# Optimization experiments

Measured on AMD Instinct MI355X. Metric: run time of the kernel, lower is better.

The kernel has to match this reference:

```python
import jax, jax.numpy as jnp
import numpy as np

N_NODES = 100000
N_EDGES = 1600000
N_FEAT = 128
HIDDEN = 64
N_CLASSES = 40


def setup_inputs() -> dict:
    key = jax.random.key(0)
    ks = jax.random.split(key, 4)
    x = jax.random.normal(ks[0], (N_NODES, N_FEAT), dtype=jnp.float32)
    edge_index = jax.random.randint(ks[1], (2, N_EDGES), 0, N_NODES, dtype=jnp.int64)
    # Glorot-style init like PyG GCNConv
    W1 = jax.random.normal(ks[2], (N_FEAT, HIDDEN), dtype=jnp.float32) * (1.0 / np.sqrt(N_FEAT))
    b1 = jnp.zeros((HIDDEN,), dtype=jnp.float32)
    W2 = jax.random.normal(ks[3], (HIDDEN, N_CLASSES), dtype=jnp.float32) * (1.0 / np.sqrt(HIDDEN))
    b2 = jnp.zeros((N_CLASSES,), dtype=jnp.float32)
    return {"x": x, "edge_index": edge_index, "W1": W1, "b1": b1, "W2": W2, "b2": b2}


def _gcn_conv(x, src, dst, norm, W, b, n_nodes):
    # PyG GCNConv: transform first, then normalized scatter-add aggregation
    h = x @ W                                   # [N, out]
    msg = h[src] * norm[:, None]                # [E+N, out] gather
    out = jax.ops.segment_sum(msg, dst, num_segments=n_nodes)  # scatter-add
    return out + b


def _norm_and_loops(edge_index, n_nodes):
    # add self-loops, symmetric normalization deg^{-1/2} A_hat deg^{-1/2}
    loop = jnp.arange(n_nodes, dtype=edge_index.dtype)
    src = jnp.concatenate([edge_index[0], loop])
    dst = jnp.concatenate([edge_index[1], loop])
    deg = jax.ops.segment_sum(jnp.ones_like(dst, dtype=jnp.float32), dst, num_segments=n_nodes)
    dinv = jnp.where(deg > 0, jax.lax.rsqrt(jnp.maximum(deg, 1.0)), 0.0)
    norm = dinv[src] * dinv[dst]
    return src, dst, norm


def reference(x, edge_index, W1, b1, W2, b2):
    n_nodes = x.shape[0]
    src, dst, norm = _norm_and_loops(edge_index, n_nodes)
    h = _gcn_conv(x, src, dst, norm, W1, b1, n_nodes)
    h = jax.nn.relu(h)
    h = _gcn_conv(h, src, dst, norm, W2, b2, n_nodes)
    return jax.nn.log_softmax(h, axis=1)
```

## Files before the change

### kernel.cpp

```cpp
#include <hip/hip_runtime.h>
#include <hip/hip_bf16.h>
#include <string.h>

#define N_FEAT 128
#define HIDDEN 64
#define N_CLS  40
#define FILL_BLOCKS 2048
#define CHUNK_EDGES 1024
#define B_BITS 6
#define SRC_BITS 17

typedef __bf16 bf16x8 __attribute__((ext_vector_type(8)));
typedef float  f32x4  __attribute__((ext_vector_type(4)));

union Frag { unsigned u[4]; bf16x8 v; };

static __device__ inline int get_xcc() {
    return (int)(__builtin_amdgcn_s_getreg((3 << 11) | 20) & 7u);
}


static __device__ inline unsigned pack_bf16(float a, float b) {
    unsigned ba = __float_as_uint(a);
    unsigned bb = __float_as_uint(b);
    unsigned ra = (ba + 0x7fffu + ((ba >> 16) & 1u)) >> 16;
    unsigned rb = (bb + 0x7fffu + ((bb >> 16) & 1u)) >> 16;
    return (ra & 0xffffu) | (rb << 16);
}

static __device__ inline float2 unpack_bf16(unsigned v) {
    return make_float2(__uint_as_float(v << 16), __uint_as_float(v & 0xffff0000u));
}


__global__ void detect_layout_kernel(const int* __restrict__ ei, int* __restrict__ flag) {
    int lane = threadIdx.x;
    int v = ei[2 * lane + 1];
    unsigned long long b = __ballot(v != 0);
    if (lane == 0) flag[0] = (b == 0ull) ? 1 : 0;
}


__global__ __launch_bounds__(256) void bucket_hist_kernel(const int* __restrict__ ei,
                                                          const int* __restrict__ flag,
                                                          unsigned* __restrict__ bcnt,
                                                          int E, int nbuk) {
    __shared__ unsigned h[2048];
    for (int i = threadIdx.x; i < nbuk; i += 256) h[i] = 0u;
    __syncthreads();
    bool is64 = (flag[0] != 0);
    if (is64) {
        int idx = blockIdx.x * 256 + threadIdx.x;
        int stride2 = gridDim.x * 256 * 2;
        int Eeven = E & ~1;
        for (int e = idx * 2; e < Eeven; e += stride2) {
            uint4 dv = *(const uint4*)(ei + (size_t)2 * E + (size_t)2 * e);
            atomicAdd(&h[((int)dv.x) >> B_BITS], 1u);
            atomicAdd(&h[((int)dv.z) >> B_BITS], 1u);
        }
        for (int e = Eeven + idx; e < E; e += gridDim.x * 256) {
            int d = ei[(size_t)2 * E + (size_t)2 * e];
            atomicAdd(&h[d >> B_BITS], 1u);
        }
    } else {
        const int* dstp = ei + E;
        for (int e = blockIdx.x * 256 + threadIdx.x; e < E; e += gridDim.x * 256) {
            int d = dstp[e];
            atomicAdd(&h[d >> B_BITS], 1u);
        }
    }
    __syncthreads();
    for (int i = threadIdx.x; i < nbuk; i += 256)
        if (h[i]) atomicAdd(&bcnt[i], h[i]);
}


__global__ __launch_bounds__(512) void bucket_scan_kernel(const unsigned* __restrict__ bcnt,
                                                          unsigned* __restrict__ bbase,
                                                          unsigned* __restrict__ bcur, int nbuk) {
    __shared__ unsigned tmp[512];
    __shared__ unsigned carry;
    if (threadIdx.x == 0) carry = 0u;
    __syncthreads();
    for (int base = 0; base < nbuk; base += 512) {
        int i = base + threadIdx.x;
        unsigned v = (i < nbuk) ? bcnt[i] : 0u;
        tmp[threadIdx.x] = v;
        __syncthreads();
#pragma unroll
        for (int off = 1; off < 512; off <<= 1) {
            unsigned t = (threadIdx.x >= (unsigned)off) ? tmp[threadIdx.x - off] : 0u;
            __syncthreads();
            tmp[threadIdx.x] += t;
            __syncthreads();
        }
        unsigned excl = tmp[threadIdx.x] - v + carry;
        if (i < nbuk) {
            bbase[i] = excl;
            bcur[(size_t)i * 16] = excl;
        }
        __syncthreads();
        if (threadIdx.x == 511) carry += tmp[511];
        __syncthreads();
    }
}


static __device__ inline void fill_edge(unsigned s, int d, int blo, int bhi,
                                        unsigned* bcur, unsigned* tmpbuf) {
    int b = d >> B_BITS;
    if (b >= blo && b < bhi) {
        unsigned val = s | ((unsigned)(d & ((1 << B_BITS) - 1)) << SRC_BITS);
        unsigned slot = __hip_atomic_fetch_add(&bcur[(size_t)b * 16], 1u, __ATOMIC_RELAXED,
                                               __HIP_MEMORY_SCOPE_WORKGROUP);
        tmpbuf[slot] = val;
    }
}

__global__ __launch_bounds__(256) void fill_buckets_kernel(const int* __restrict__ ei,
                                                           const int* __restrict__ flag,
                                                           unsigned* __restrict__ bcur,
                                                           unsigned* __restrict__ ctr,
                                                           unsigned* __restrict__ tmpbuf,
                                                           int E, int nbuk) {
    int r = get_xcc();
    int bpx = (nbuk + 7) >> 3;
    int blo = r * bpx;
    int bhi = min(nbuk, blo + bpx);
    bool is64 = (flag[0] != 0);
    const int* dstp = is64 ? (ei + 2 * E) : (ei + E);
    int stride = is64 ? 2 : 1;
    __shared__ unsigned chunk_s;
    for (;;) {
        if (threadIdx.x == 0)
            chunk_s = __hip_atomic_fetch_add(&ctr[r * 64], 1u, __ATOMIC_RELAXED,
                                             __HIP_MEMORY_SCOPE_WORKGROUP);
        __syncthreads();
        long long base = (long long)chunk_s * CHUNK_EDGES;
        __syncthreads();
        if (base >= E) break;
        if (is64 && base + CHUNK_EDGES <= E) {
            int e0 = (int)base + threadIdx.x * 2;
            int e1 = e0 + 512;
            uint4 sA = *(const uint4*)(ei + (size_t)2 * e0);
            uint4 sB = *(const uint4*)(ei + (size_t)2 * e1);
            uint4 dA = *(const uint4*)(ei + (size_t)2 * E + (size_t)2 * e0);
            uint4 dB = *(const uint4*)(ei + (size_t)2 * E + (size_t)2 * e1);
            fill_edge(sA.x, (int)dA.x, blo, bhi, bcur, tmpbuf);
            fill_edge(sA.z, (int)dA.z, blo, bhi, bcur, tmpbuf);
            fill_edge(sB.x, (int)dB.x, blo, bhi, bcur, tmpbuf);
            fill_edge(sB.z, (int)dB.z, blo, bhi, bcur, tmpbuf);
        } else {
            int end = (int)min((long long)E, base + CHUNK_EDGES);
            for (int e = (int)base + threadIdx.x; e < end; e += 256) {
                int d = dstp[(size_t)e * stride];
                int b = d >> B_BITS;
                if (b >= blo && b < bhi) {
                    int s = ei[(size_t)e * stride];
                    unsigned val = (unsigned)s | ((unsigned)(d & ((1 << B_BITS) - 1)) << SRC_BITS);
                    unsigned slot = __hip_atomic_fetch_add(&bcur[(size_t)b * 16], 1u, __ATOMIC_RELAXED,
                                                           __HIP_MEMORY_SCOPE_WORKGROUP);
                    tmpbuf[slot] = val;
                }
            }
        }
    }
}


__global__ __launch_bounds__(256) void bucket_to_csr_kernel(const unsigned* __restrict__ tmpbuf,
                                                            const unsigned* __restrict__ bbase,
                                                            unsigned* __restrict__ deg,
                                                            unsigned* __restrict__ rowptr,
                                                            float* __restrict__ dinv,
                                                            int* __restrict__ csr_src,
                                                            int nbuk, int N, int E) {
    int b = blockIdx.x;
    int tid = threadIdx.x;
    unsigned beg = bbase[b];
    unsigned end = (b + 1 < nbuk) ? bbase[b + 1] : (unsigned)E;
    int d0 = b << B_BITS;
    const int ND = 1 << B_BITS;
    __shared__ unsigned hist[ND], scn[ND], cur[ND];
    if (tid < ND) { hist[tid] = 0u; cur[tid] = 0u; }
    __syncthreads();
    for (unsigned i = beg + tid; i < end; i += 256)
        atomicAdd(&hist[tmpbuf[i] >> SRC_BITS], 1u);
    __syncthreads();
    if (tid == 0) {
        unsigned run = 0;
        for (int k = 0; k < ND; ++k) { scn[k] = run; run += hist[k]; }
    }
    __syncthreads();
    if (tid < ND) {
        int d = d0 + tid;
        if (d < N) {
            unsigned dg = hist[tid];
            deg[d] = dg;
            dinv[d] = rsqrtf((float)(dg + 1u));
            rowptr[d] = beg + scn[tid];
        }
    }
    __syncthreads();
    for (unsigned i = beg + tid; i < end; i += 256) {
        unsigned v = tmpbuf[i];
        unsigned dl = v >> SRC_BITS;
        unsigned s = v & ((1u << SRC_BITS) - 1u);
        unsigned p = atomicAdd(&cur[dl], 1u);
        csr_src[beg + scn[dl] + p] = (int)s;
    }
}


__global__ __launch_bounds__(256) void gemm1_mfma_kernel(const float* __restrict__ x,
                                                         const float* __restrict__ W1,
                                                         unsigned* __restrict__ h1b, int N) {
    int lane = threadIdx.x & 63;
    int quad = lane >> 4;
    int col  = lane & 15;

    Frag B[4][4];
#pragma unroll
    for (int c = 0; c < 4; ++c)
#pragma unroll
        for (int ks = 0; ks < 4; ++ks) {
            int n = c * 16 + col;
#pragma unroll
            for (int jj = 0; jj < 4; ++jj) {
                int k = ks * 32 + quad * 8 + 2 * jj;
                B[c][ks].u[jj] = pack_bf16(W1[k * HIDDEN + n], W1[(k + 1) * HIDDEN + n]);
            }
        }

    int wave_id = blockIdx.x * 4 + (threadIdx.x >> 6);
    int nwaves  = gridDim.x * 4;
    int ntiles  = (N + 15) >> 4;

    for (int rt = wave_id; rt < ntiles; rt += nwaves) {
        int rowA = rt * 16 + col;
        Frag A[4];
#pragma unroll
        for (int ks = 0; ks < 4; ++ks) {
            float4 a0 = make_float4(0.f, 0.f, 0.f, 0.f), a1 = a0;
            if (rowA < N) {
                const float4* ap = (const float4*)(x + (size_t)rowA * N_FEAT + ks * 32 + quad * 8);
                a0 = ap[0];
                a1 = ap[1];
            }
            A[ks].u[0] = pack_bf16(a0.x, a0.y);
            A[ks].u[1] = pack_bf16(a0.z, a0.w);
            A[ks].u[2] = pack_bf16(a1.x, a1.y);
            A[ks].u[3] = pack_bf16(a1.z, a1.w);
        }
        f32x4 acc[4] = {{0.f, 0.f, 0.f, 0.f}, {0.f, 0.f, 0.f, 0.f},
                        {0.f, 0.f, 0.f, 0.f}, {0.f, 0.f, 0.f, 0.f}};
#pragma unroll
        for (int ks = 0; ks < 4; ++ks)
#pragma unroll
            for (int c = 0; c < 4; ++c)
                acc[c] = __builtin_amdgcn_mfma_f32_16x16x32_bf16(A[ks].v, B[c][ks].v, acc[c], 0, 0, 0);

        int rowD = rt * 16 + quad * 4;
#pragma unroll
        for (int c = 0; c < 4; ++c)
#pragma unroll
            for (int r = 0; r < 4; ++r) {
                float v = acc[c][r];
                float nxt = __shfl_down(v, 1);
                int row = rowD + r;
                if (((lane & 1) == 0) && row < N)
                    h1b[(size_t)row * 32 + ((c * 16 + col) >> 1)] = pack_bf16(v, nxt);
            }
    }
}


__global__ __launch_bounds__(256) void gemm2_mfma_kernel(const unsigned* __restrict__ actb,
                                                         const float* __restrict__ W2,
                                                         unsigned* __restrict__ h2b, int N) {
    int lane = threadIdx.x & 63;
    int quad = lane >> 4;
    int col  = lane & 15;

    Frag B[3][2];
#pragma unroll
    for (int c = 0; c < 3; ++c)
#pragma unroll
        for (int ks = 0; ks < 2; ++ks) {
            int n = c * 16 + col;
#pragma unroll
            for (int jj = 0; jj < 4; ++jj) {
                int k = ks * 32 + quad * 8 + 2 * jj;
                float w0 = (n < N_CLS) ? W2[k * N_CLS + n] : 0.f;
                float w1 = (n < N_CLS) ? W2[(k + 1) * N_CLS + n] : 0.f;
                B[c][ks].u[jj] = pack_bf16(w0, w1);
            }
        }

    int wave_id = blockIdx.x * 4 + (threadIdx.x >> 6);
    int nwaves  = gridDim.x * 4;
    int ntiles  = (N + 15) >> 4;

    for (int rt = wave_id; rt < ntiles; rt += nwaves) {
        int rowA = rt * 16 + col;
        Frag A[2];
#pragma unroll
        for (int ks = 0; ks < 2; ++ks) {
            uint4 u = make_uint4(0u, 0u, 0u, 0u);
            if (rowA < N)
                u = *(const uint4*)(actb + (size_t)rowA * 32 + ks * 16 + quad * 4);
            A[ks].u[0] = u.x; A[ks].u[1] = u.y; A[ks].u[2] = u.z; A[ks].u[3] = u.w;
        }
        f32x4 acc[3] = {{0.f, 0.f, 0.f, 0.f}, {0.f, 0.f, 0.f, 0.f}, {0.f, 0.f, 0.f, 0.f}};
#pragma unroll
        for (int ks = 0; ks < 2; ++ks)
#pragma unroll
            for (int c = 0; c < 3; ++c)
                acc[c] = __builtin_amdgcn_mfma_f32_16x16x32_bf16(A[ks].v, B[c][ks].v, acc[c], 0, 0, 0);

        int rowD = rt * 16 + quad * 4;
#pragma unroll
        for (int c = 0; c < 3; ++c)
#pragma unroll
            for (int r = 0; r < 4; ++r) {
                float v = acc[c][r];
                float nxt = __shfl_down(v, 1);
                int row = rowD + r;
                int pair = (c * 16 + col) >> 1;
                if (((lane & 1) == 0) && pair < 20 && row < N)
                    h2b[(size_t)row * 20 + pair] = pack_bf16(v, nxt);
            }
    }
}


__global__ __launch_bounds__(256) void agg1_kernel(const unsigned* __restrict__ h1b,
                                                   const int* __restrict__ csr_src,
                                                   const unsigned* __restrict__ rowptr,
                                                   const unsigned* __restrict__ deg,
                                                   const float* __restrict__ dinv,
                                                   const float* __restrict__ b1,
                                                   unsigned* __restrict__ actb, int N) {
    int wave = threadIdx.x >> 6, lane = threadIdx.x & 63;
    int sub = lane >> 5, j = lane & 31;
    int d = blockIdx.x * 4 + wave;
    if (d >= N) return;
    float dv = dinv[d];
    float acc0 = 0.f, acc1 = 0.f;
    if (sub == 0) {
        float2 v = unpack_bf16(h1b[(size_t)d * 32 + j]);
        acc0 = dv * v.x; acc1 = dv * v.y;
    }
    unsigned beg = rowptr[d];
    int len = (int)deg[d];
    int i = 0;
    for (; i + 8 <= len; i += 8) {
        int s0 = csr_src[beg + i + sub];
        int s1 = csr_src[beg + i + 2 + sub];
        int s2 = csr_src[beg + i + 4 + sub];
        int s3 = csr_src[beg + i + 6 + sub];
        float w0 = dinv[s0], w1 = dinv[s1], w2 = dinv[s2], w3 = dinv[s3];
        unsigned v0 = h1b[(size_t)s0 * 32 + j];
        unsigned v1 = h1b[(size_t)s1 * 32 + j];
        unsigned v2 = h1b[(size_t)s2 * 32 + j];
        unsigned v3 = h1b[(size_t)s3 * 32 + j];
        float2 a0 = unpack_bf16(v0), a1 = unpack_bf16(v1);
        float2 a2 = unpack_bf16(v2), a3 = unpack_bf16(v3);
        acc0 += w0 * a0.x + w1 * a1.x + w2 * a2.x + w3 * a3.x;
        acc1 += w0 * a0.y + w1 * a1.y + w2 * a2.y + w3 * a3.y;
    }
    for (; i + 4 <= len; i += 4) {
        int sA = csr_src[beg + i + sub];
        int sB = csr_src[beg + i + 2 + sub];
        float wA = dinv[sA], wB = dinv[sB];
        float2 a = unpack_bf16(h1b[(size_t)sA * 32 + j]);
        float2 b = unpack_bf16(h1b[(size_t)sB * 32 + j]);
        acc0 += wA * a.x + wB * b.x;
        acc1 += wA * a.y + wB * b.y;
    }
    for (; i < len; i += 2) {
        int e = i + sub;
        if (e < len) {
            int s = csr_src[beg + e];
            float w = dinv[s];
            float2 a = unpack_bf16(h1b[(size_t)s * 32 + j]);
            acc0 += w * a.x;
            acc1 += w * a.y;
        }
    }
    acc0 += __shfl_xor(acc0, 32);
    acc1 += __shfl_xor(acc1, 32);
    if (sub == 0) {
        float2 bb = ((const float2*)b1)[j];
        float r0 = fmaxf(acc0 * dv + bb.x, 0.f);
        float r1 = fmaxf(acc1 * dv + bb.y, 0.f);
        actb[(size_t)d * 32 + j] = pack_bf16(r0, r1);
    }
}


__global__ __launch_bounds__(256) void agg2_lsm_kernel(const unsigned* __restrict__ h2b,
                                                       const int* __restrict__ csr_src,
                                                       const unsigned* __restrict__ rowptr,
                                                       const unsigned* __restrict__ deg,
                                                       const float* __restrict__ dinv,
                                                       const float* __restrict__ b2,
                                                       float* __restrict__ out, int N) {
    int wave = threadIdx.x >> 6, lane = threadIdx.x & 63;
    int sub = lane >> 5, j = lane & 31;
    bool act = (j < 20);
    int d = blockIdx.x * 4 + wave;
    if (d >= N) return;
    float dv = dinv[d];
    float acc0 = 0.f, acc1 = 0.f;
    if (sub == 0 && act) {
        float2 v = unpack_bf16(h2b[(size_t)d * 20 + j]);
        acc0 = dv * v.x; acc1 = dv * v.y;
    }
    unsigned beg = rowptr[d];
    int len = (int)deg[d];
    int i = 0;
    for (; i + 8 <= len; i += 8) {
        int s0 = csr_src[beg + i + sub];
        int s1 = csr_src[beg + i + 2 + sub];
        int s2 = csr_src[beg + i + 4 + sub];
        int s3 = csr_src[beg + i + 6 + sub];
        float w0 = dinv[s0], w1 = dinv[s1], w2 = dinv[s2], w3 = dinv[s3];
        if (act) {
            float2 a0 = unpack_bf16(h2b[(size_t)s0 * 20 + j]);
            float2 a1 = unpack_bf16(h2b[(size_t)s1 * 20 + j]);
            float2 a2 = unpack_bf16(h2b[(size_t)s2 * 20 + j]);
            float2 a3 = unpack_bf16(h2b[(size_t)s3 * 20 + j]);
            acc0 += w0 * a0.x + w1 * a1.x + w2 * a2.x + w3 * a3.x;
            acc1 += w0 * a0.y + w1 * a1.y + w2 * a2.y + w3 * a3.y;
        }
    }
    for (; i + 4 <= len; i += 4) {
        int sA = csr_src[beg + i + sub];
        int sB = csr_src[beg + i + 2 + sub];
        float wA = dinv[sA], wB = dinv[sB];
        if (act) {
            float2 a = unpack_bf16(h2b[(size_t)sA * 20 + j]);
            float2 b = unpack_bf16(h2b[(size_t)sB * 20 + j]);
            acc0 += wA * a.x + wB * b.x;
            acc1 += wA * a.y + wB * b.y;
        }
    }
    for (; i < len; i += 2) {
        int e = i + sub;
        if (e < len && act) {
            int s = csr_src[beg + e];
            float w = dinv[s];
            float2 a = unpack_bf16(h2b[(size_t)s * 20 + j]);
            acc0 += w * a.x;
            acc1 += w * a.y;
        }
    }
    acc0 += __shfl_xor(acc0, 32);
    acc1 += __shfl_xor(acc1, 32);
    float v0 = -1e30f, v1 = -1e30f;
    if (act) {
        float2 bb = ((const float2*)b2)[j];
        v0 = acc0 * dv + bb.x;
        v1 = acc1 * dv + bb.y;
    }
    float m = fmaxf(v0, v1);
#pragma unroll
    for (int off = 32; off > 0; off >>= 1)
        m = fmaxf(m, __shfl_xor(m, off));
    float ex = (act && sub == 0) ? (expf(v0 - m) + expf(v1 - m)) : 0.f;
#pragma unroll
    for (int off = 32; off > 0; off >>= 1)
        ex += __shfl_xor(ex, off);
    float ls = logf(ex);
    if (act && sub == 0) {
        float2* orow = (float2*)(out + (size_t)d * N_CLS);
        orow[j] = make_float2(v0 - m - ls, v1 - m - ls);
    }
}


static inline size_t align_up(size_t x) { return (x + 255) & ~(size_t)255; }

extern "C" void kernel_launch(void* const* d_in, const int* in_sizes, int n_in,
                              void* d_out, int out_size, void* d_ws, size_t ws_size,
                              hipStream_t stream) {
    const float* x  = (const float*)d_in[0];
    const int*   ei = (const int*)d_in[1];
    const float* W1 = (const float*)d_in[2];
    const float* b1 = (const float*)d_in[3];
    const float* W2 = (const float*)d_in[4];
    const float* b2 = (const float*)d_in[5];

    int N = in_sizes[0] / N_FEAT;
    int E = in_sizes[1] / 2;
    int nbuk = (N + (1 << B_BITS) - 1) >> B_BITS;

    char* ws = (char*)d_ws;
    int*      flag    = (int*)ws;       ws += 256;
    unsigned* ctrs    = (unsigned*)ws;  ws += 4096;
    unsigned* bcnt    = (unsigned*)ws;  ws += align_up((size_t)nbuk * 4);
    unsigned* bbase   = (unsigned*)ws;  ws += align_up((size_t)nbuk * 4);
    unsigned* bcur    = (unsigned*)ws;  ws += align_up((size_t)nbuk * 64);
    unsigned* deg     = (unsigned*)ws;  ws += align_up((size_t)N * 4);
    float*    dinv    = (float*)ws;     ws += align_up((size_t)N * 4);
    unsigned* rowptr  = (unsigned*)ws;  ws += align_up((size_t)N * 4);
    unsigned* tmpbuf  = (unsigned*)ws;  ws += align_up((size_t)E * 4);
    int*      csr_src = (int*)ws;       ws += align_up((size_t)E * 4);
    unsigned* h1b     = (unsigned*)ws;  ws += align_up((size_t)N * 32 * 4);
    unsigned* actb    = (unsigned*)ws;  ws += align_up((size_t)N * 32 * 4);
    unsigned* h2b     = (unsigned*)ws;  ws += align_up((size_t)N * 20 * 4);

    hipMemsetAsync(ctrs, 0, 4096, stream);
    hipMemsetAsync(bcnt, 0, (size_t)nbuk * 4, stream);

    detect_layout_kernel<<<1, 64, 0, stream>>>(ei, flag);
    bucket_hist_kernel<<<256, 256, 0, stream>>>(ei, flag, bcnt, E, nbuk);
    bucket_scan_kernel<<<1, 512, 0, stream>>>(bcnt, bbase, bcur, nbuk);
    fill_buckets_kernel<<<FILL_BLOCKS, 256, 0, stream>>>(ei, flag, bcur, ctrs, tmpbuf, E, nbuk);
    bucket_to_csr_kernel<<<nbuk, 256, 0, stream>>>(tmpbuf, bbase, deg, rowptr, dinv, csr_src, nbuk, N, E);

    gemm1_mfma_kernel<<<512, 256, 0, stream>>>(x, W1, h1b, N);
    agg1_kernel<<<(N + 3) / 4, 256, 0, stream>>>(h1b, csr_src, rowptr, deg, dinv, b1, actb, N);

    gemm2_mfma_kernel<<<512, 256, 0, stream>>>(actb, W2, h2b, N);
    agg2_lsm_kernel<<<(N + 3) / 4, 256, 0, stream>>>(h2b, csr_src, rowptr, deg, dinv, b2, (float*)d_out, N);
}
```

Baseline: 354.2 us.

## Stage owned edges in LDS and batch bucket atomics per chunk in fill kernel

The bucket fill kernel now takes much larger edge chunks and stages each XCC's owned edges in shared memory. It builds a per-bucket histogram in LDS, then issues one global atomic per bucket per chunk instead of one per edge, and scatters from the stage to tmpbuf. The aim is fewer global atomics and more grouped writes to tmpbuf. In exchange it adds LDS pressure, extra barriers and a fallback path with per-edge atomics when the stage overflows. The larger chunks may also leave load imbalance across blocks.

```diff
diff --git a/kernel.cpp b/kernel.cpp
--- a/kernel.cpp
+++ b/kernel.cpp
@@ -5,8 +5,9 @@
 #define N_FEAT 128
 #define HIDDEN 64
 #define N_CLS  40
-#define FILL_BLOCKS 2048
-#define CHUNK_EDGES 1024
+#define FILL_BLOCKS 1024
+#define CHUNK_EDGES 16384
+#define STAGE_CAP 6144
 #define B_BITS 6
 #define SRC_BITS 17
 
@@ -105,17 +106,6 @@
     }
 }
 
-
-static __device__ inline void fill_edge(unsigned s, int d, int blo, int bhi,
-                                        unsigned* bcur, unsigned* tmpbuf) {
-    int b = d >> B_BITS;
-    if (b >= blo && b < bhi) {
-        unsigned val = s | ((unsigned)(d & ((1 << B_BITS) - 1)) << SRC_BITS);
-        unsigned slot = __hip_atomic_fetch_add(&bcur[(size_t)b * 16], 1u, __ATOMIC_RELAXED,
-                                               __HIP_MEMORY_SCOPE_WORKGROUP);
-        tmpbuf[slot] = val;
-    }
-}
 
 __global__ __launch_bounds__(256) void fill_buckets_kernel(const int* __restrict__ ei,
                                                            const int* __restrict__ flag,
@@ -127,43 +117,114 @@
     int bpx = (nbuk + 7) >> 3;
     int blo = r * bpx;
     int bhi = min(nbuk, blo + bpx);
+    int nlb = bhi - blo;
     bool is64 = (flag[0] != 0);
-    const int* dstp = is64 ? (ei + 2 * E) : (ei + E);
-    int stride = is64 ? 2 : 1;
-    __shared__ unsigned chunk_s;
+    const size_t dstoff = (size_t)2 * E;
+
+    __shared__ unsigned stage[STAGE_CAP];
+    __shared__ unsigned hist[256], lbase[256], lcur[256];
+    __shared__ unsigned tail_s, chunk_s;
+
+    int lane = threadIdx.x & 63;
+    unsigned long long lmask_lt = (lane == 0) ? 0ull : ((~0ull) >> (64 - lane));
+
+    auto stage_edge = [&](bool own, unsigned v, unsigned lb) {
+        unsigned long long mask = __ballot(own ? 1 : 0);
+        int cnt = __popcll(mask);
+        if (cnt) {
+            unsigned bp = 0;
+            int leader = __builtin_ctzll(mask);
+            if (lane == leader) bp = atomicAdd(&tail_s, (unsigned)cnt);
+            bp = __shfl(bp, leader);
+            if (own) {
+                unsigned pos = bp + (unsigned)__popcll(mask & lmask_lt);
+                if (pos < STAGE_CAP) {
+                    stage[pos] = v;
+                    atomicAdd(&hist[lb], 1u);
+                } else {
+                    unsigned slot = __hip_atomic_fetch_add(&bcur[(size_t)(blo + (int)lb) * 16], 1u,
+                                                           __ATOMIC_RELAXED, __HIP_MEMORY_SCOPE_WORKGROUP);
+                    tmpbuf[slot] = v & 0x7fffffu;
+                }
+            }
+        }
+    };
+
     for (;;) {
-        if (threadIdx.x == 0)
+        if (threadIdx.x == 0) {
             chunk_s = __hip_atomic_fetch_add(&ctr[r * 64], 1u, __ATOMIC_RELAXED,
                                              __HIP_MEMORY_SCOPE_WORKGROUP);
+            tail_s = 0u;
+        }
+        if (threadIdx.x < 256) { hist[threadIdx.x] = 0u; lcur[threadIdx.x] = 0u; }
         __syncthreads();
         long long base = (long long)chunk_s * CHUNK_EDGES;
-        __syncthreads();
         if (base >= E) break;
-        if (is64 && base + CHUNK_EDGES <= E) {
-            int e0 = (int)base + threadIdx.x * 2;
-            int e1 = e0 + 512;
-            uint4 sA = *(const uint4*)(ei + (size_t)2 * e0);
-            uint4 sB = *(const uint4*)(ei + (size_t)2 * e1);
-            uint4 dA = *(const uint4*)(ei + (size_t)2 * E + (size_t)2 * e0);
-            uint4 dB = *(const uint4*)(ei + (size_t)2 * E + (size_t)2 * e1);
-            fill_edge(sA.x, (int)dA.x, blo, bhi, bcur, tmpbuf);
-            fill_edge(sA.z, (int)dA.z, blo, bhi, bcur, tmpbuf);
-            fill_edge(sB.x, (int)dB.x, blo, bhi, bcur, tmpbuf);
-            fill_edge(sB.z, (int)dB.z, blo, bhi, bcur, tmpbuf);
+        int end = (int)min((long long)E, base + CHUNK_EDGES);
+
+        if (is64) {
+            for (int e = (int)base + 2 * threadIdx.x; e + 1 < end; e += 512) {
+                uint4 sv = *(const uint4*)(ei + (size_t)2 * e);
+                uint4 dv = *(const uint4*)(ei + dstoff + (size_t)2 * e);
+                {
+                    int d = (int)dv.x;
+                    int b = d >> B_BITS;
+                    bool own = (b >= blo && b < bhi);
+                    unsigned lb = own ? (unsigned)(b - blo) : 0u;
+                    unsigned v = (lb << 23) | ((unsigned)(d & ((1 << B_BITS) - 1)) << SRC_BITS) | sv.x;
+                    stage_edge(own, v, lb);
+                }
+                {
+                    int d = (int)dv.z;
+                    int b = d >> B_BITS;
+                    bool own = (b >= blo && b < bhi);
+                    unsigned lb = own ? (unsigned)(b - blo) : 0u;
+                    unsigned v = (lb << 23) | ((unsigned)(d & ((1 << B_BITS) - 1)) << SRC_BITS) | sv.z;
+                    stage_edge(own, v, lb);
+                }
+            }
+            if ((end - (int)base) & 1) {
+                bool own = false; unsigned v = 0, lb = 0;
+                if (threadIdx.x == 0) {
+                    int e = end - 1;
+                    int d = ei[dstoff + (size_t)2 * e];
+                    int b = d >> B_BITS;
+                    if (b >= blo && b < bhi) {
+                        own = true; lb = (unsigned)(b - blo);
+                        v = (lb << 23) | ((unsigned)(d & ((1 << B_BITS) - 1)) << SRC_BITS)
+                            | (unsigned)ei[(size_t)2 * e];
+                    }
+                }
+                stage_edge(own, v, lb);
+            }
         } else {
-            int end = (int)min((long long)E, base + CHUNK_EDGES);
             for (int e = (int)base + threadIdx.x; e < end; e += 256) {
-                int d = dstp[(size_t)e * stride];
+                int d = ei[(size_t)E + e];
                 int b = d >> B_BITS;
-                if (b >= blo && b < bhi) {
-                    int s = ei[(size_t)e * stride];
-                    unsigned val = (unsigned)s | ((unsigned)(d & ((1 << B_BITS) - 1)) << SRC_BITS);
-                    unsigned slot = __hip_atomic_fetch_add(&bcur[(size_t)b * 16], 1u, __ATOMIC_RELAXED,
-                                                           __HIP_MEMORY_SCOPE_WORKGROUP);
-                    tmpbuf[slot] = val;
-                }
-            }
-        }
+                bool own = (b >= blo && b < bhi);
+                unsigned lb = own ? (unsigned)(b - blo) : 0u;
+                unsigned v = (lb << 23) | ((unsigned)(d & ((1 << B_BITS) - 1)) << SRC_BITS)
+                             | (own ? (unsigned)ei[e] : 0u);
+                stage_edge(own, v, lb);
+            }
+        }
+        __syncthreads();
+
+        for (int lb = threadIdx.x; lb < nlb; lb += 256) {
+            unsigned h = hist[lb];
+            if (h) lbase[lb] = __hip_atomic_fetch_add(&bcur[(size_t)(blo + lb) * 16], h,
+                                                      __ATOMIC_RELAXED, __HIP_MEMORY_SCOPE_WORKGROUP);
+        }
+        __syncthreads();
+
+        unsigned tl = min(tail_s, (unsigned)STAGE_CAP);
+        for (unsigned i = threadIdx.x; i < tl; i += 256) {
+            unsigned v = stage[i];
+            unsigned lb = v >> 23;
+            unsigned off = atomicAdd(&lcur[lb], 1u);
+            tmpbuf[lbase[lb] + off] = v & 0x7fffffu;
+        }
+        __syncthreads();
     }
 }
 
```

Result: faster. 321.8 us (-9.2%).
